# Kernel optimization log

Measured on AMD Instinct MI355X. Metric: run time of the kernel, lower is better.

Reference implementation:

```python
import jax, jax.numpy as jnp
import numpy as np

N = 50000          # num_entities
R = 16             # num_relations
D = 128            # embedding_dim
B = 4              # num_blocks
d = D // B         # block size (32)
E = 800000         # num edges


def setup_inputs() -> dict:
    key = jax.random.key(0)
    ks = jax.random.split(key, 9)
    s = 1.0 / np.sqrt(D)
    return {
        "edge_index": jax.random.randint(ks[0], (2, E), 0, N),
        "edge_type": jax.random.randint(ks[1], (E,), 0, R),
        "node_emb": jax.random.normal(ks[2], (N, D), jnp.float32) * s,
        "W1": jax.random.normal(ks[3], (R, B, d, d), jnp.float32) * s,
        "root1": jax.random.normal(ks[4], (D, D), jnp.float32) * s,
        "bias1": jax.random.normal(ks[5], (D,), jnp.float32) * 0.01,
        "W2": jax.random.normal(ks[6], (R, B, d, d), jnp.float32) * s,
        "root2": jax.random.normal(ks[7], (D, D), jnp.float32) * s,
        "bias2": jax.random.normal(ks[8], (D,), jnp.float32) * 0.01,
    }


def _rgcn_conv(x, src, dst, et, W, root, bias):
    # x: [N, D]; W: [R, B, d, d] block-diagonal per-relation weights.
    n = x.shape[0]
    # Transform every node under every relation (cheaper than gathering
    # per-edge weight blocks): [R, N, B, d] -> [R, N, D]
    allR = jnp.einsum('nbi,rbio->rnbo', x.reshape(n, B, d), W).reshape(R, n, D)
    msg = allR[et, src]                                   # [E, D] gather
    # Per-relation mean normalization 1/c_{i,r} (PyG RGCNConv aggr='mean'
    # applied per relation): count edges per (dst, relation) pair.
    seg = dst * R + et
    cnt = jax.ops.segment_sum(jnp.ones_like(et, x.dtype), seg, num_segments=n * R)
    norm = 1.0 / jnp.maximum(cnt[seg], 1.0)               # [E]
    agg = jax.ops.segment_sum(msg * norm[:, None], dst, num_segments=n)
    return agg + x @ root + bias


def reference(edge_index, edge_type, node_emb, W1, root1, bias1, W2, root2, bias2):
    src, dst = edge_index[0], edge_index[1]
    h = _rgcn_conv(node_emb, src, dst, edge_type, W1, root1, bias1)
    h = jax.nn.relu(h)  # dropout is identity in eval mode
    return _rgcn_conv(h, src, dst, edge_type, W2, root2, bias2)
```

## Files before the change

kernel.cpp:

```cpp
#include <hip/hip_runtime.h>
#include <hip/hip_bf16.h>

#define N_NODES 50000
#define N_REL   16
#define DIM     128
#define NBLK    4
#define BS      32
#define N_EDGES 800000
#define NSEG    (N_NODES * N_REL)
#define SCAN_BLK 1024
#define N_SCAN_BLKS ((NSEG + SCAN_BLK - 1) / SCAN_BLK)
#define NWT     (N_NODES / 16)

typedef __attribute__((ext_vector_type(8))) short s8v;
typedef __attribute__((ext_vector_type(8))) unsigned short u8v;
typedef __attribute__((ext_vector_type(4))) float f4v;

__device__ __forceinline__ float bf2f(unsigned short u) {
    return __uint_as_float(((unsigned int)u) << 16);
}
__device__ __forceinline__ unsigned short f2bfbits(float f) {
    unsigned int u = __float_as_uint(f);
    return (unsigned short)((u + 0x7fffu + ((u >> 16) & 1u)) >> 16);
}

__global__ __launch_bounds__(256) void count_kernel(const int* __restrict__ dst,
                                                    const int* __restrict__ et,
                                                    int* __restrict__ cnt, int E) {
    int e = blockIdx.x * 256 + threadIdx.x;
    if (e < E) atomicAdd(&cnt[dst[e] * N_REL + et[e]], 1);
}

__global__ __launch_bounds__(256) void scan1_kernel(const int* __restrict__ in,
                                                    int* __restrict__ out,
                                                    int* __restrict__ bsum, int M) {
    const int t = threadIdx.x;
    const int base = blockIdx.x * SCAN_BLK + t * 4;
    int v0 = (base + 0 < M) ? in[base + 0] : 0;
    int v1 = (base + 1 < M) ? in[base + 1] : 0;
    int v2 = (base + 2 < M) ? in[base + 2] : 0;
    int v3 = (base + 3 < M) ? in[base + 3] : 0;
    const int s = v0 + v1 + v2 + v3;
    const int lane = t & 63, wid = t >> 6;
    int inc = s;
    for (int d = 1; d < 64; d <<= 1) {
        int u = __shfl_up(inc, d, 64);
        if (lane >= d) inc += u;
    }
    __shared__ int wsum[5];
    if (lane == 63) wsum[wid] = inc;
    __syncthreads();
    if (t == 0) {
        int a = 0;
        for (int w = 0; w < 4; ++w) { int u = wsum[w]; wsum[w] = a; a += u; }
        wsum[4] = a;
    }
    __syncthreads();
    const int ex = inc - s + wsum[wid];
    if (base + 0 < M) out[base + 0] = ex;
    if (base + 1 < M) out[base + 1] = ex + v0;
    if (base + 2 < M) out[base + 2] = ex + v0 + v1;
    if (base + 3 < M) out[base + 3] = ex + v0 + v1 + v2;
    if (t == 0) bsum[blockIdx.x] = wsum[4];
}

__global__ __launch_bounds__(1024) void scan2_kernel(int* __restrict__ bsum, int nb) {
    const int t = threadIdx.x;
    int s = (t < nb) ? bsum[t] : 0;
    const int lane = t & 63, wid = t >> 6;
    int inc = s;
    for (int d = 1; d < 64; d <<= 1) {
        int u = __shfl_up(inc, d, 64);
        if (lane >= d) inc += u;
    }
    __shared__ int wsum[16];
    if (lane == 63) wsum[wid] = inc;
    __syncthreads();
    if (t == 0) {
        int a = 0;
        for (int w = 0; w < 16; ++w) { int u = wsum[w]; wsum[w] = a; a += u; }
    }
    __syncthreads();
    const int ex = inc - s + wsum[wid];
    if (t < nb) bsum[t] = ex;
}

__global__ __launch_bounds__(256) void scan3_kernel(int* __restrict__ out,
                                                    const int* __restrict__ bsum, int M) {
    int i = blockIdx.x * 256 + threadIdx.x;
    if (i < M) out[i] += bsum[i / SCAN_BLK];
}

__global__ __launch_bounds__(256) void scatter_fast_kernel(const int* __restrict__ src,
                                                           const int* __restrict__ dst,
                                                           const int* __restrict__ et,
                                                           int* __restrict__ off,
                                                           const int* __restrict__ cnt,
                                                           int2* __restrict__ evec, int E) {
    int e = blockIdx.x * 256 + threadIdx.x;
    if (e < E) {
        int r = et[e];
        int seg = dst[e] * N_REL + r;
        int pos = atomicAdd(&off[seg], 1);
        float inv = 1.0f / (float)cnt[seg];
        evec[pos] = make_int2(r * N_NODES + src[e], __float_as_int(inv));
    }
}

__global__ __launch_bounds__(256) void scatter_old_kernel(const int* __restrict__ src,
                                                          const int* __restrict__ dst,
                                                          const int* __restrict__ et,
                                                          int* __restrict__ off,
                                                          int* __restrict__ srcs, int E) {
    int e = blockIdx.x * 256 + threadIdx.x;
    if (e < E) {
        int seg = dst[e] * N_REL + et[e];
        int pos = atomicAdd(&off[seg], 1);
        srcs[pos] = src[e];
    }
}

__global__ __launch_bounds__(256) void prep_kernel(const float* __restrict__ W1,
                                                   const float* __restrict__ W2,
                                                   const float* __restrict__ r1,
                                                   const float* __restrict__ r2,
                                                   ushort* __restrict__ WB1,
                                                   ushort* __restrict__ WB2,
                                                   ushort* __restrict__ RB1,
                                                   ushort* __restrict__ RB2) {
    int t = blockIdx.x * 256 + threadIdx.x;
    if (t < 262144) {
        const float* W = (t < 131072) ? W1 : W2;
        ushort* WB     = (t < 131072) ? WB1 : WB2;
        int idx = t & 131071;
        int i  = idx & 7;
        int lm = (idx >> 3) & 15;
        int kg = (idx >> 7) & 3;
        int mt = (idx >> 9) & 1;
        int b  = (idx >> 10) & 3;
        int r  = idx >> 12;
        WB[idx] = f2bfbits(W[((size_t)(r * 4 + b) * 32 + kg * 8 + i) * 32 + mt * 16 + lm]);
    } else if (t < 294912) {
        int u = t - 262144;
        const float* R = (u < 16384) ? r1 : r2;
        ushort* RB     = (u < 16384) ? RB1 : RB2;
        int idx = u & 16383;
        int i  = idx & 7;
        int lm = (idx >> 3) & 15;
        int kg = (idx >> 7) & 3;
        int kc = (idx >> 9) & 3;
        int mt = (idx >> 11) & 7;
        RB[idx] = f2bfbits(R[(size_t)(kc * 32 + kg * 8 + i) * DIM + mt * 16 + lm]);
    }
}

template<bool IN_BF16, bool OUT_BF16, bool RELU>
__global__ __launch_bounds__(256) void fused_kernel(const void* __restrict__ xin,
                                                    const ushort* __restrict__ WB,
                                                    const ushort* __restrict__ RB,
                                                    const float* __restrict__ bias,
                                                    char* __restrict__ tab,
                                                    float* __restrict__ scl,
                                                    void* __restrict__ outv) {
    const int wv = threadIdx.x >> 6;
    const int l  = threadIdx.x & 63;
    const int wt = blockIdx.x * 4 + wv;
    if (wt >= NWT) return;
    const int rbase = blockIdx.y * 8;
    const int nbase = wt * 16;
    const int lm = l & 15;
    const int kg = l >> 4;
    const int node = nbase + lm;

    s8v bfr[4];
#pragma unroll
    for (int b = 0; b < 4; ++b) {
        if (IN_BF16) {
            const ushort* xp = (const ushort*)xin + (size_t)node * DIM + b * BS + kg * 8;
            u8v u = *(const u8v*)xp;
#pragma unroll
            for (int i = 0; i < 8; ++i) {
                unsigned short us = u[i];
                if (RELU) us = (us & 0x8000u) ? (unsigned short)0 : us;
                bfr[b][i] = (short)us;
            }
        } else {
            const float* xp = (const float*)xin + (size_t)node * DIM + b * BS + kg * 8;
#pragma unroll
            for (int i = 0; i < 8; ++i) {
                float v = xp[i];
                if (RELU) v = fmaxf(v, 0.f);
                bfr[b][i] = (short)f2bfbits(v);
            }
        }
    }

#pragma unroll 2
    for (int ri = 0; ri < 8; ++ri) {
        const int rr = rbase + ri;
        f4v acc[4][2];
#pragma unroll
        for (int b = 0; b < 4; ++b) {
#pragma unroll
            for (int mt = 0; mt < 2; ++mt) {
                s8v afrag = *(const s8v*)&WB[((((rr * 4 + b) * 2 + mt) * 4 + kg) * 16 + lm) * 8];
                f4v z = {0.f, 0.f, 0.f, 0.f};
                acc[b][mt] = __builtin_amdgcn_mfma_f32_16x16x32_bf16(afrag, bfr[b], z, 0, 0, 0);
            }
        }
        float m = 0.f;
#pragma unroll
        for (int b = 0; b < 4; ++b)
#pragma unroll
            for (int mt = 0; mt < 2; ++mt)
#pragma unroll
                for (int j = 0; j < 4; ++j)
                    m = fmaxf(m, fabsf(acc[b][mt][j]));
        m = fmaxf(m, __shfl_xor(m, 16, 64));
        m = fmaxf(m, __shfl_xor(m, 32, 64));
        m = fmaxf(m, 1e-30f);
        const float qs = 127.0f / m;

        unsigned int d[8];
#pragma unroll
        for (int b = 0; b < 4; ++b) {
#pragma unroll
            for (int mt = 0; mt < 2; ++mt) {
                int q0 = __float2int_rn(acc[b][mt][0] * qs);
                int q1 = __float2int_rn(acc[b][mt][1] * qs);
                int q2 = __float2int_rn(acc[b][mt][2] * qs);
                int q3 = __float2int_rn(acc[b][mt][3] * qs);
                unsigned int t01 = __builtin_amdgcn_perm((unsigned)q1, (unsigned)q0, 0x00000400u);
                unsigned int t23 = __builtin_amdgcn_perm((unsigned)q3, (unsigned)q2, 0x00000400u);
                d[b * 2 + mt] = __builtin_amdgcn_perm(t23, t01, 0x05040100u);
            }
        }
        char* gp = tab + ((size_t)rr * N_NODES + node) * 128 + kg * 32;
        *(uint4*)gp        = make_uint4(d[0], d[1], d[2], d[3]);
        *(uint4*)(gp + 16) = make_uint4(d[4], d[5], d[6], d[7]);
        if (kg == 0) scl[rr * N_NODES + node] = m * (1.0f / 127.0f);
    }

    if (blockIdx.y == 0) {
#pragma unroll 2
        for (int mt = 0; mt < 8; ++mt) {
            const int col0 = mt * 16 + kg * 4;
            f4v acc = *(const f4v*)&bias[col0];
#pragma unroll
            for (int kc = 0; kc < 4; ++kc) {
                s8v afrag = *(const s8v*)&RB[(((mt * 4 + kc) * 4 + kg) * 16 + lm) * 8];
                acc = __builtin_amdgcn_mfma_f32_16x16x32_bf16(afrag, bfr[kc], acc, 0, 0, 0);
            }
            if (OUT_BF16) {
                unsigned int p0 = (unsigned int)f2bfbits(acc[0]) |
                                  ((unsigned int)f2bfbits(acc[1]) << 16);
                unsigned int p1 = (unsigned int)f2bfbits(acc[2]) |
                                  ((unsigned int)f2bfbits(acc[3]) << 16);
                *(uint2*)((ushort*)outv + (size_t)node * DIM + col0) = make_uint2(p0, p1);
            } else {
                *(f4v*)((float*)outv + (size_t)node * DIM + col0) = acc;
            }
        }
    }
}

template<bool OUT_BF16>
__global__ __launch_bounds__(256) void agg8_kernel(const int2* __restrict__ evec,
                                                   const int* __restrict__ off,
                                                   const char* __restrict__ tab,
                                                   const float* __restrict__ scl,
                                                   void* __restrict__ outv) {
    const int hw = threadIdx.x >> 5;
    const int o  = threadIdx.x & 31;
    const int v  = blockIdx.x * 8 + hw;

    const int start = (v == 0) ? 0 : off[v * N_REL - 1];
    const int end   = off[v * N_REL + N_REL - 1];

    const int p = o >> 4;
    const int w = o & 15;

    float acc[8];
#pragma unroll
    for (int j = 0; j < 8; ++j) acc[j] = 0.f;

#pragma unroll 2
    for (int base = start; base < end; base += 4) {
        const int k0 = base + p;
        const int k1 = base + 2 + p;
        const int2 e0 = evec[min(k0, end - 1)];
        const int2 e1 = evec[min(k1, end - 1)];
        const int g0 = e0.x, g1 = e1.x;
        const float i0 = (k0 < end) ? __int_as_float(e0.y) : 0.f;
        const float i1 = (k1 < end) ? __int_as_float(e1.y) : 0.f;
        const uint2 q0 = *(const uint2*)(tab + (size_t)g0 * 128 + w * 8);
        const uint2 q1 = *(const uint2*)(tab + (size_t)g1 * 128 + w * 8);
        const float s0 = scl[g0] * i0;
        const float s1 = scl[g1] * i1;
#pragma unroll
        for (int j = 0; j < 4; ++j) {
            acc[j]     = fmaf((float)(int)(signed char)(q0.x >> (8 * j)), s0, acc[j]);
            acc[4 + j] = fmaf((float)(int)(signed char)(q0.y >> (8 * j)), s0, acc[4 + j]);
        }
#pragma unroll
        for (int j = 0; j < 4; ++j) {
            acc[j]     = fmaf((float)(int)(signed char)(q1.x >> (8 * j)), s1, acc[j]);
            acc[4 + j] = fmaf((float)(int)(signed char)(q1.y >> (8 * j)), s1, acc[4 + j]);
        }
    }
#pragma unroll
    for (int j = 0; j < 8; ++j)
        acc[j] += __shfl_xor(acc[j], 16, 32);

    if (o < 16) {
        const int base0 = (o & 3) * 32 + (o >> 2) * 4;
        if (OUT_BF16) {
            ushort* hp = (ushort*)outv + (size_t)v * DIM + base0;
            ushort4 a0 = *(ushort4*)hp;
            ushort4 a1 = *(ushort4*)(hp + 16);
            a0.x = f2bfbits(bf2f(a0.x) + acc[0]);
            a0.y = f2bfbits(bf2f(a0.y) + acc[1]);
            a0.z = f2bfbits(bf2f(a0.z) + acc[2]);
            a0.w = f2bfbits(bf2f(a0.w) + acc[3]);
            a1.x = f2bfbits(bf2f(a1.x) + acc[4]);
            a1.y = f2bfbits(bf2f(a1.y) + acc[5]);
            a1.z = f2bfbits(bf2f(a1.z) + acc[6]);
            a1.w = f2bfbits(bf2f(a1.w) + acc[7]);
            *(ushort4*)hp        = a0;
            *(ushort4*)(hp + 16) = a1;
        } else {
            float* op = (float*)outv + (size_t)v * DIM + base0;
            float4 r0 = *(float4*)op;
            float4 r1 = *(float4*)(op + 16);
            r0.x += acc[0]; r0.y += acc[1]; r0.z += acc[2]; r0.w += acc[3];
            r1.x += acc[4]; r1.y += acc[5]; r1.z += acc[6]; r1.w += acc[7];
            *(float4*)op        = r0;
            *(float4*)(op + 16) = r1;
        }
    }
}

template<bool RELU>
__global__ __launch_bounds__(256) void dense_old_kernel(const float* __restrict__ x,
                                                        const float* __restrict__ root,
                                                        const float* __restrict__ bias,
                                                        float* __restrict__ out) {
    const int wv = threadIdx.x >> 6;
    const int l  = threadIdx.x & 63;
    const int wt = blockIdx.x * 4 + wv;
    if (wt >= NWT) return;
    const int nbase = wt * 16;
    const int lm = l & 15;
    const int kg = l >> 4;
    const int node = nbase + lm;

    s8v bfr[4];
#pragma unroll
    for (int kc = 0; kc < 4; ++kc) {
        const float* xp = &x[(size_t)node * DIM + kc * BS + kg * 8];
#pragma unroll
        for (int i = 0; i < 8; ++i) {
            float v = xp[i];
            if (RELU) v = fmaxf(v, 0.f);
            bfr[kc][i] = (short)f2bfbits(v);
        }
    }
#pragma unroll 2
    for (int mt = 0; mt < 8; ++mt) {
        const int col0 = mt * 16 + kg * 4;
        f4v acc = *(const f4v*)&bias[col0];
#pragma unroll
        for (int kc = 0; kc < 4; ++kc) {
            const float* rp = &root[(size_t)(kc * BS + kg * 8) * DIM + mt * 16 + lm];
            s8v afrag;
#pragma unroll
            for (int i = 0; i < 8; ++i)
                afrag[i] = (short)f2bfbits(rp[i * DIM]);
            acc = __builtin_amdgcn_mfma_f32_16x16x32_bf16(afrag, bfr[kc], acc, 0, 0, 0);
        }
        *(f4v*)&out[(size_t)node * DIM + col0] = acc;
    }
}

template<bool RELU>
__global__ __launch_bounds__(256) void agg_fallback_kernel(const int* __restrict__ srcs,
                                                           const int* __restrict__ off,
                                                           const int* __restrict__ cnt,
                                                           const float* __restrict__ x,
                                                           const float* __restrict__ W,
                                                           float* __restrict__ out) {
    __shared__ float Wsh[N_REL * BS * BS];
    const int bblk = blockIdx.y;
    for (int idx = threadIdx.x * 4; idx < N_REL * BS * BS; idx += 1024) {
        int r = idx >> 10, rest = idx & 1023;
        *(float4*)&Wsh[idx] = *(const float4*)&W[(r * NBLK + bblk) * 1024 + rest];
    }
    __syncthreads();
    const int hw = threadIdx.x >> 5;
    const int o  = threadIdx.x & 31;
    const int v  = blockIdx.x * 8 + hw;
    int endv = 0, cv = 0;
    if (o < N_REL) { endv = off[v * N_REL + o]; cv = cnt[v * N_REL + o]; }
    float acc = out[v * DIM + bblk * BS + o];
    for (int r = 0; r < N_REL; ++r) {
        const int c = __shfl(cv, r, 32);
        if (c == 0) continue;
        const int end = __shfl(endv, r, 32);
        float xs = 0.f;
        for (int k = end - c; k < end; ++k) {
            const int s = srcs[k];
            float xv = x[s * DIM + bblk * BS + o];
            if (RELU) xv = fmaxf(xv, 0.f);
            xs += xv;
        }
        xs *= (1.0f / (float)c);
        const float* wr = &Wsh[r * (BS * BS)];
#pragma unroll
        for (int i = 0; i < BS; i += 2) {
            float xi0 = __shfl(xs, i, 32);
            float xi1 = __shfl(xs, i + 1, 32);
            acc = fmaf(xi0, wr[i * BS + o], acc);
            acc = fmaf(xi1, wr[(i + 1) * BS + o], acc);
        }
    }
    out[v * DIM + bblk * BS + o] = acc;
}

extern "C" void kernel_launch(void* const* d_in, const int* in_sizes, int n_in,
                              void* d_out, int out_size, void* d_ws, size_t ws_size,
                              hipStream_t stream) {
    const int*   edge_index = (const int*)d_in[0];
    const int*   src   = edge_index;
    const int*   dstv  = edge_index + N_EDGES;
    const int*   et    = (const int*)d_in[1];
    const float* x0    = (const float*)d_in[2];
    const float* W1    = (const float*)d_in[3];
    const float* root1 = (const float*)d_in[4];
    const float* bias1 = (const float*)d_in[5];
    const float* W2    = (const float*)d_in[6];
    const float* root2 = (const float*)d_in[7];
    const float* bias2 = (const float*)d_in[8];
    float* out = (float*)d_out;

    char* ws = (char*)d_ws;
    ushort* h    = (ushort*)ws;
    int*    cnt  = (int*)   (ws + 12800000);
    int*    off  = (int*)   (ws + 16000000);
    int2*   evec = (int2*)  (ws + 19200000);
    int*    bsum = (int*)   (ws + 25600000);
    ushort* WB1  = (ushort*)(ws + 25604096);
    ushort* WB2  = (ushort*)(ws + 25866240);
    ushort* RB1  = (ushort*)(ws + 26128384);
    ushort* RB2  = (ushort*)(ws + 26161152);
    float*  scl  = (float*) (ws + 26193920);
    char*   tab  =          (ws + 29393920);
    const size_t FAST_NEED = 131793920ull;

    const int egrid = (N_EDGES + 255) / 256;
    const int tgrid = (NWT + 3) / 4;

    if (ws_size >= FAST_NEED) {
        prep_kernel<<<1152, 256, 0, stream>>>(W1, W2, root1, root2, WB1, WB2, RB1, RB2);
        hipMemsetAsync(cnt, 0, (size_t)NSEG * sizeof(int), stream);
        count_kernel<<<egrid, 256, 0, stream>>>(dstv, et, cnt, N_EDGES);
        scan1_kernel<<<N_SCAN_BLKS, 256, 0, stream>>>(cnt, off, bsum, NSEG);
        scan2_kernel<<<1, 1024, 0, stream>>>(bsum, N_SCAN_BLKS);
        scan3_kernel<<<(NSEG + 255) / 256, 256, 0, stream>>>(off, bsum, NSEG);
        scatter_fast_kernel<<<egrid, 256, 0, stream>>>(src, dstv, et, off, cnt, evec, N_EDGES);

        dim3 fgrid(tgrid, 2);
        const int ngrid = N_NODES / 8;

        fused_kernel<false, true, false><<<fgrid, 256, 0, stream>>>(
            x0, WB1, RB1, bias1, tab, scl, h);
        agg8_kernel<true><<<ngrid, 256, 0, stream>>>(evec, off, tab, scl, h);

        fused_kernel<true, false, true><<<fgrid, 256, 0, stream>>>(
            h, WB2, RB2, bias2, tab, scl, out);
        agg8_kernel<false><<<ngrid, 256, 0, stream>>>(evec, off, tab, scl, out);
    } else {
        float* hf    = (float*)d_ws;
        int*   cntf  = (int*)((char*)d_ws + 25600000);
        int*   offf  = (int*)((char*)d_ws + 28800000);
        int*   srcsf = (int*)((char*)d_ws + 32000000);
        int*   bsumf = (int*)((char*)d_ws + 35200000);

        hipMemsetAsync(cntf, 0, (size_t)NSEG * sizeof(int), stream);
        count_kernel<<<egrid, 256, 0, stream>>>(dstv, et, cntf, N_EDGES);
        scan1_kernel<<<N_SCAN_BLKS, 256, 0, stream>>>(cntf, offf, bsumf, NSEG);
        scan2_kernel<<<1, 1024, 0, stream>>>(bsumf, N_SCAN_BLKS);
        scan3_kernel<<<(NSEG + 255) / 256, 256, 0, stream>>>(offf, bsumf, NSEG);
        scatter_old_kernel<<<egrid, 256, 0, stream>>>(src, dstv, et, offf, srcsf, N_EDGES);

        dim3 fgrid2(N_NODES / 8, NBLK);
        dense_old_kernel<false><<<tgrid, 256, 0, stream>>>(x0, root1, bias1, hf);
        agg_fallback_kernel<false><<<fgrid2, 256, 0, stream>>>(srcsf, offf, cntf, x0, W1, hf);
        dense_old_kernel<true><<<tgrid, 256, 0, stream>>>(hf, root2, bias2, out);
        agg_fallback_kernel<true><<<fgrid2, 256, 0, stream>>>(srcsf, offf, cntf, hf, W2, out);
    }
}
```

Before: 248.7 us.

## Compact transformed-message table to only (relation, source) pairs used by edges

Marks which (relation, source node) pairs appear as edge sources, prefix-scans those flags alongside the segment counts to get compact indices, and makes the fused transform kernel write quantized int8 rows and scales only for used pairs into a compacted table. Edge records now store the compact index. This cuts table write traffic and shrinks the gather footprint, which may improve cache hit rate during aggregation. The cost is an extra scattered store per edge, a second scanned array, and extra used/cmap loads in the transform kernel. The fused kernel still computes the MFMAs for every pair.

```diff
diff --git a/kernel.cpp b/kernel.cpp
--- a/kernel.cpp
+++ b/kernel.cpp
@@ -24,11 +24,116 @@
     return (unsigned short)((u + 0x7fffu + ((u >> 16) & 1u)) >> 16);
 }
 
-__global__ __launch_bounds__(256) void count_kernel(const int* __restrict__ dst,
+__global__ __launch_bounds__(256) void count_kernel(const int* __restrict__ src,
+                                                    const int* __restrict__ dst,
                                                     const int* __restrict__ et,
-                                                    int* __restrict__ cnt, int E) {
+                                                    int* __restrict__ cnt,
+                                                    int* __restrict__ used, int E) {
     int e = blockIdx.x * 256 + threadIdx.x;
-    if (e < E) atomicAdd(&cnt[dst[e] * N_REL + et[e]], 1);
+    if (e < E) {
+        int r = et[e];
+        atomicAdd(&cnt[dst[e] * N_REL + r], 1);
+        used[r * N_NODES + src[e]] = 1;
+    }
+}
+
+__global__ __launch_bounds__(256) void scan1j_kernel(const int* __restrict__ cnt,
+                                                     const int* __restrict__ used,
+                                                     int* __restrict__ off,
+                                                     int* __restrict__ cmap,
+                                                     int2* __restrict__ bsum, int M) {
+    const int t = threadIdx.x;
+    const int base = blockIdx.x * SCAN_BLK + t * 4;
+    int c[4], u[4];
+#pragma unroll
+    for (int i = 0; i < 4; ++i) {
+        int idx = base + i;
+        c[i] = (idx < M) ? cnt[idx] : 0;
+        u[i] = (idx < M) ? used[idx] : 0;
+    }
+    int cs = c[0] + c[1] + c[2] + c[3];
+    int us = u[0] + u[1] + u[2] + u[3];
+    const int lane = t & 63, wid = t >> 6;
+    int cinc = cs, uinc = us;
+    for (int d = 1; d < 64; d <<= 1) {
+        int a = __shfl_up(cinc, d, 64);
+        int b = __shfl_up(uinc, d, 64);
+        if (lane >= d) { cinc += a; uinc += b; }
+    }
+    __shared__ int cw[5], uw[5];
+    if (lane == 63) { cw[wid] = cinc; uw[wid] = uinc; }
+    __syncthreads();
+    if (t == 0) {
+        int a = 0, b = 0;
+        for (int w = 0; w < 4; ++w) {
+            int x = cw[w]; cw[w] = a; a += x;
+            int y = uw[w]; uw[w] = b; b += y;
+        }
+        cw[4] = a; uw[4] = b;
+    }
+    __syncthreads();
+    int cex = cinc - cs + cw[wid];
+    int uex = uinc - us + uw[wid];
+#pragma unroll
+    for (int i = 0; i < 4; ++i) {
+        int idx = base + i;
+        if (idx < M) { off[idx] = cex; cmap[idx] = uex; }
+        cex += c[i]; uex += u[i];
+    }
+    if (t == 0) bsum[blockIdx.x] = make_int2(cw[4], uw[4]);
+}
+
+__global__ __launch_bounds__(1024) void scan2j_kernel(int2* __restrict__ bsum, int nb) {
+    const int t = threadIdx.x;
+    int2 s = (t < nb) ? bsum[t] : make_int2(0, 0);
+    const int lane = t & 63, wid = t >> 6;
+    int ci = s.x, ui = s.y;
+    for (int d = 1; d < 64; d <<= 1) {
+        int a = __shfl_up(ci, d, 64);
+        int b = __shfl_up(ui, d, 64);
+        if (lane >= d) { ci += a; ui += b; }
+    }
+    __shared__ int cw[16], uw[16];
+    if (lane == 63) { cw[wid] = ci; uw[wid] = ui; }
+    __syncthreads();
+    if (t == 0) {
+        int a = 0, b = 0;
+        for (int w = 0; w < 16; ++w) {
+            int x = cw[w]; cw[w] = a; a += x;
+            int y = uw[w]; uw[w] = b; b += y;
+        }
+    }
+    __syncthreads();
+    if (t < nb) bsum[t] = make_int2(ci - s.x + cw[wid], ui - s.y + uw[wid]);
+}
+
+__global__ __launch_bounds__(256) void scan3j_kernel(int* __restrict__ off,
+                                                     int* __restrict__ cmap,
+                                                     const int2* __restrict__ bsum, int M) {
+    int i = blockIdx.x * 256 + threadIdx.x;
+    if (i < M) {
+        int2 b = bsum[i / SCAN_BLK];
+        off[i] += b.x;
+        cmap[i] += b.y;
+    }
+}
+
+__global__ __launch_bounds__(256) void scatter_fast_kernel(const int* __restrict__ src,
+                                                           const int* __restrict__ dst,
+                                                           const int* __restrict__ et,
+                                                           int* __restrict__ off,
+                                                           const int* __restrict__ cnt,
+                                                           const int* __restrict__ cmap,
+                                                           int2* __restrict__ evec, int E) {
+    int e = blockIdx.x * 256 + threadIdx.x;
+    if (e < E) {
+        int r = et[e];
+        int seg = dst[e] * N_REL + r;
+        int pos = atomicAdd(&off[seg], 1);
+        float inv = 1.0f / (float)cnt[seg];
+        int g = cmap[r * N_NODES + src[e]];
+        evec[pos] = make_int2(g, __float_as_int(inv));
+    }
 }
 
 __global__ __launch_bounds__(256) void scan1_kernel(const int* __restrict__ in,
@@ -89,22 +194,6 @@
                                                     const int* __restrict__ bsum, int M) {
     int i = blockIdx.x * 256 + threadIdx.x;
     if (i < M) out[i] += bsum[i / SCAN_BLK];
-}
-
-__global__ __launch_bounds__(256) void scatter_fast_kernel(const int* __restrict__ src,
-                                                           const int* __restrict__ dst,
-                                                           const int* __restrict__ et,
-                                                           int* __restrict__ off,
-                                                           const int* __restrict__ cnt,
-                                                           int2* __restrict__ evec, int E) {
-    int e = blockIdx.x * 256 + threadIdx.x;
-    if (e < E) {
-        int r = et[e];
-        int seg = dst[e] * N_REL + r;
-        int pos = atomicAdd(&off[seg], 1);
-        float inv = 1.0f / (float)cnt[seg];
-        evec[pos] = make_int2(r * N_NODES + src[e], __float_as_int(inv));
-    }
 }
 
 __global__ __launch_bounds__(256) void scatter_old_kernel(const int* __restrict__ src,
@@ -159,6 +248,8 @@
                                                     const ushort* __restrict__ WB,
                                                     const ushort* __restrict__ RB,
                                                     const float* __restrict__ bias,
+                                                    const int* __restrict__ used,
+                                                    const int* __restrict__ cmap,
                                                     char* __restrict__ tab,
                                                     float* __restrict__ scl,
                                                     void* __restrict__ outv) {
@@ -198,6 +289,9 @@
 #pragma unroll 2
     for (int ri = 0; ri < 8; ++ri) {
         const int rr = rbase + ri;
+        const int grow = rr * N_NODES + node;
+        const int flag = used[grow];
+        const int cid  = cmap[grow];
         f4v acc[4][2];
 #pragma unroll
         for (int b = 0; b < 4; ++b) {
@@ -219,26 +313,28 @@
         m = fmaxf(m, __shfl_xor(m, 16, 64));
         m = fmaxf(m, __shfl_xor(m, 32, 64));
         m = fmaxf(m, 1e-30f);
-        const float qs = 127.0f / m;
-
-        unsigned int d[8];
-#pragma unroll
-        for (int b = 0; b < 4; ++b) {
-#pragma unroll
-            for (int mt = 0; mt < 2; ++mt) {
-                int q0 = __float2int_rn(acc[b][mt][0] * qs);
-                int q1 = __float2int_rn(acc[b][mt][1] * qs);
-                int q2 = __float2int_rn(acc[b][mt][2] * qs);
-                int q3 = __float2int_rn(acc[b][mt][3] * qs);
-                unsigned int t01 = __builtin_amdgcn_perm((unsigned)q1, (unsigned)q0, 0x00000400u);
-                unsigned int t23 = __builtin_amdgcn_perm((unsigned)q3, (unsigned)q2, 0x00000400u);
-                d[b * 2 + mt] = __builtin_amdgcn_perm(t23, t01, 0x05040100u);
+
+        if (flag) {
+            const float qs = 127.0f / m;
+            unsigned int d[8];
+#pragma unroll
+            for (int b = 0; b < 4; ++b) {
+#pragma unroll
+                for (int mt = 0; mt < 2; ++mt) {
+                    int q0 = __float2int_rn(acc[b][mt][0] * qs);
+                    int q1 = __float2int_rn(acc[b][mt][1] * qs);
+                    int q2 = __float2int_rn(acc[b][mt][2] * qs);
+                    int q3 = __float2int_rn(acc[b][mt][3] * qs);
+                    unsigned int t01 = __builtin_amdgcn_perm((unsigned)q1, (unsigned)q0, 0x00000400u);
+                    unsigned int t23 = __builtin_amdgcn_perm((unsigned)q3, (unsigned)q2, 0x00000400u);
+                    d[b * 2 + mt] = __builtin_amdgcn_perm(t23, t01, 0x05040100u);
+                }
             }
-        }
-        char* gp = tab + ((size_t)rr * N_NODES + node) * 128 + kg * 32;
-        *(uint4*)gp        = make_uint4(d[0], d[1], d[2], d[3]);
-        *(uint4*)(gp + 16) = make_uint4(d[4], d[5], d[6], d[7]);
-        if (kg == 0) scl[rr * N_NODES + node] = m * (1.0f / 127.0f);
+            char* gp = tab + (size_t)cid * 128 + kg * 32;
+            *(uint4*)gp        = make_uint4(d[0], d[1], d[2], d[3]);
+            *(uint4*)(gp + 16) = make_uint4(d[4], d[5], d[6], d[7]);
+            if (kg == 0) scl[cid] = m * (1.0f / 127.0f);
+        }
     }
 
     if (blockIdx.y == 0) {
@@ -445,38 +541,41 @@
     char* ws = (char*)d_ws;
     ushort* h    = (ushort*)ws;
     int*    cnt  = (int*)   (ws + 12800000);
-    int*    off  = (int*)   (ws + 16000000);
-    int2*   evec = (int2*)  (ws + 19200000);
-    int*    bsum = (int*)   (ws + 25600000);
-    ushort* WB1  = (ushort*)(ws + 25604096);
-    ushort* WB2  = (ushort*)(ws + 25866240);
-    ushort* RB1  = (ushort*)(ws + 26128384);
-    ushort* RB2  = (ushort*)(ws + 26161152);
-    float*  scl  = (float*) (ws + 26193920);
-    char*   tab  =          (ws + 29393920);
-    const size_t FAST_NEED = 131793920ull;
+    int*    used = (int*)   (ws + 16000000);
+    int*    off  = (int*)   (ws + 19200000);
+    int*    cmap = (int*)   (ws + 22400000);
+    int2*   evec = (int2*)  (ws + 25600000);
+    int2*   bsum = (int2*)  (ws + 32000000);
+    ushort* WB1  = (ushort*)(ws + 32008192);
+    ushort* WB2  = (ushort*)(ws + 32270336);
+    ushort* RB1  = (ushort*)(ws + 32532480);
+    ushort* RB2  = (ushort*)(ws + 32565248);
+    float*  scl  = (float*) (ws + 32598016);
+    char*   tab  =          (ws + 35798016);
+    const size_t FAST_NEED = 138198016ull;
 
     const int egrid = (N_EDGES + 255) / 256;
     const int tgrid = (NWT + 3) / 4;
 
     if (ws_size >= FAST_NEED) {
         prep_kernel<<<1152, 256, 0, stream>>>(W1, W2, root1, root2, WB1, WB2, RB1, RB2);
-        hipMemsetAsync(cnt, 0, (size_t)NSEG * sizeof(int), stream);
-        count_kernel<<<egrid, 256, 0, stream>>>(dstv, et, cnt, N_EDGES);
-        scan1_kernel<<<N_SCAN_BLKS, 256, 0, stream>>>(cnt, off, bsum, NSEG);
-        scan2_kernel<<<1, 1024, 0, stream>>>(bsum, N_SCAN_BLKS);
-        scan3_kernel<<<(NSEG + 255) / 256, 256, 0, stream>>>(off, bsum, NSEG);
-        scatter_fast_kernel<<<egrid, 256, 0, stream>>>(src, dstv, et, off, cnt, evec, N_EDGES);
+        hipMemsetAsync(cnt, 0, 2 * (size_t)NSEG * sizeof(int), stream);
+        count_kernel<<<egrid, 256, 0, stream>>>(src, dstv, et, cnt, used, N_EDGES);
+        scan1j_kernel<<<N_SCAN_BLKS, 256, 0, stream>>>(cnt, used, off, cmap, bsum, NSEG);
+        scan2j_kernel<<<1, 1024, 0, stream>>>(bsum, N_SCAN_BLKS);
+        scan3j_kernel<<<(NSEG + 255) / 256, 256, 0, stream>>>(off, cmap, bsum, NSEG);
+        scatter_fast_kernel<<<egrid, 256, 0, stream>>>(src, dstv, et, off, cnt, cmap,
+                                                       evec, N_EDGES);
 
         dim3 fgrid(tgrid, 2);
         const int ngrid = N_NODES / 8;
 
         fused_kernel<false, true, false><<<fgrid, 256, 0, stream>>>(
-            x0, WB1, RB1, bias1, tab, scl, h);
+            x0, WB1, RB1, bias1, used, cmap, tab, scl, h);
         agg8_kernel<true><<<ngrid, 256, 0, stream>>>(evec, off, tab, scl, h);
 
         fused_kernel<true, false, true><<<fgrid, 256, 0, stream>>>(
-            h, WB2, RB2, bias2, tab, scl, out);
+            h, WB2, RB2, bias2, used, cmap, tab, scl, out);
         agg8_kernel<false><<<ngrid, 256, 0, stream>>>(evec, off, tab, scl, out);
     } else {
         float* hf    = (float*)d_ws;
@@ -484,9 +583,10 @@
         int*   offf  = (int*)((char*)d_ws + 28800000);
         int*   srcsf = (int*)((char*)d_ws + 32000000);
         int*   bsumf = (int*)((char*)d_ws + 35200000);
+        int*   usedD = offf;
 
         hipMemsetAsync(cntf, 0, (size_t)NSEG * sizeof(int), stream);
-        count_kernel<<<egrid, 256, 0, stream>>>(dstv, et, cntf, N_EDGES);
+        count_kernel<<<egrid, 256, 0, stream>>>(src, dstv, et, cntf, usedD, N_EDGES);
         scan1_kernel<<<N_SCAN_BLKS, 256, 0, stream>>>(cntf, offf, bsumf, NSEG);
         scan2_kernel<<<1, 1024, 0, stream>>>(bsumf, N_SCAN_BLKS);
         scan3_kernel<<<(NSEG + 255) / 256, 256, 0, stream>>>(offf, bsumf, NSEG);
```

New measurement: 246.2 us. Within noise of the previous version (-1.0%).
